# Kernel optimization log

Measured on AMD Instinct MI355X. Metric: run time of the kernel, lower is better.

The kernel has to match this reference:

```python
import jax, jax.numpy as jnp
import numpy as np

AUG_DIMS = 8
ODE_STEPS = 20  # fixed-step RK4 over t in [0, 1]


def _augment(x):
    # concat zeros along last (channel) dim: [B, S, F] -> [B, S, F + AUG_DIMS]
    z = jnp.zeros(x.shape[:-1] + (AUG_DIMS,), dtype=x.dtype)
    return jnp.concatenate([x, z], axis=-1)


def _ode_solve(z0, W, b):
    # dz/dt = z @ W.T + b, integrated with RK4, 20 steps, t: 0 -> 1
    h = 1.0 / ODE_STEPS

    def f(z):
        return z @ W.T + b

    def step(z, _):
        k1 = f(z)
        k2 = f(z + 0.5 * h * k1)
        k3 = f(z + 0.5 * h * k2)
        k4 = f(z + h * k3)
        z = z + (h / 6.0) * (k1 + 2.0 * k2 + 2.0 * k3 + k4)
        return z, None

    z_final, _ = jax.lax.scan(step, z0, None, length=ODE_STEPS)
    return z_final


def setup_inputs() -> dict:
    key = jax.random.key(0)
    ks = jax.random.split(key, 7)
    F_, C_, H_ = 76, 5, 128
    D = F_ + AUG_DIMS  # 84
    x = jax.random.normal(ks[0], (32, 2048, F_), dtype=jnp.float32)
    s = 1.0 / np.sqrt(D)
    W_ode = jax.random.uniform(ks[1], (D, D), minval=-s, maxval=s, dtype=jnp.float32)
    b_ode = jax.random.uniform(ks[2], (D,), minval=-s, maxval=s, dtype=jnp.float32)
    W_pen = jax.random.uniform(ks[3], (H_, D), minval=-s, maxval=s, dtype=jnp.float32)
    b_pen = jax.random.uniform(ks[4], (H_,), minval=-s, maxval=s, dtype=jnp.float32)
    sh = 1.0 / np.sqrt(H_)
    W_fin = jax.random.uniform(ks[5], (C_, H_), minval=-sh, maxval=sh, dtype=jnp.float32)
    b_fin = jax.random.uniform(ks[6], (C_,), minval=-sh, maxval=sh, dtype=jnp.float32)
    return {"x": x, "W_ode": W_ode, "b_ode": b_ode, "W_pen": W_pen,
            "b_pen": b_pen, "W_fin": W_fin, "b_fin": b_fin}


def reference(x, W_ode, b_ode, W_pen, b_pen, W_fin, b_fin):
    z0 = _augment(x)                       # [B, S, 84]
    z = _ode_solve(z0, W_ode, b_ode)       # ODE solve
    z = z + z0                             # skip-add of augmented input
    h = jax.nn.relu(z @ W_pen.T + b_pen)   # [B, S, 128]
    return h @ W_fin.T + b_fin             # [B, S, 5]
```

## Files before the change

### kernel.cpp

```cpp
#include <hip/hip_runtime.h>

#define K_IN 76
#define DD 84
#define HCH 128
#define CCH 5

#define OFF_U 0
#define OFF_C (K_IN*HCH)

__device__ __constant__ float CU[9] = {
    1.f, 0.5f, 1.f/6.f, 1.f/24.f, 1.f/120.f, 1.f/720.f, 1.f/5040.f,
    1.f/40320.f, 1.f/362880.f };
__device__ __constant__ float CC[9] = {
    0.5f, 1.f/6.f, 1.f/24.f, 1.f/120.f, 1.f/720.f, 1.f/5040.f,
    1.f/40320.f, 1.f/362880.f, 1.f/3628800.f };

__global__ __launch_bounds__(64, 1) void col_kernel(
    const float* __restrict__ W,
    const float* __restrict__ bode,
    const float* __restrict__ Wpen,
    const float* __restrict__ bpen,
    float* __restrict__ ws)
{
    __shared__ __align__(16) float Sa[88];
    __shared__ __align__(16) float Sb[88];

    const int l  = threadIdx.x;
    const int j  = blockIdx.x;
    const int i2 = 64 + l;
    const bool has2 = (l < 20);

    float wc1[DD], wc2[DD];
#pragma unroll
    for (int k = 0; k < DD; ++k) wc1[k] = W[k*DD + l];
    if (has2) {
#pragma unroll
        for (int k = 0; k < DD; ++k) wc2[k] = W[k*DD + i2];
    }

    float s1 = Wpen[j*DD + l];
    float s2 = has2 ? Wpen[j*DD + i2] : 0.f;
    const float b1 = bode[l];
    const float b2 = has2 ? bode[i2] : 0.f;

    Sa[l] = s1;
    if (has2) Sa[i2] = s2;
    __threadfence_block();

    float u1 = 2.f*s1, c1 = s1;
    float u2 = 2.f*s2, c2 = s2;

    const float* Sc = Sa;
    float*       Sn = Sb;
#pragma unroll
    for (int n = 0; n < 9; ++n) {
        float a0 = 0.f, a1 = 0.f, a2 = 0.f, a3 = 0.f;
        float e0 = 0.f, e1 = 0.f, e2 = 0.f, e3 = 0.f;
#pragma unroll
        for (int mg = 0; mg < 21; ++mg) {
            const float4 sv = *(const float4*)&Sc[mg*4];
            a0 = fmaf(sv.x, wc1[mg*4+0], a0);
            a1 = fmaf(sv.y, wc1[mg*4+1], a1);
            a2 = fmaf(sv.z, wc1[mg*4+2], a2);
            a3 = fmaf(sv.w, wc1[mg*4+3], a3);
            e0 = fmaf(sv.x, wc2[mg*4+0], e0);
            e1 = fmaf(sv.y, wc2[mg*4+1], e1);
            e2 = fmaf(sv.z, wc2[mg*4+2], e2);
            e3 = fmaf(sv.w, wc2[mg*4+3], e3);
        }
        const float d1 = (a0 + a1) + (a2 + a3);
        const float d2 = (e0 + e1) + (e2 + e3);

        Sn[l] = d1;
        if (has2) Sn[i2] = d2;
        __threadfence_block();

        u1 = fmaf(CU[n], d1, u1);  c1 = fmaf(CC[n], d1, c1);
        u2 = fmaf(CU[n], d2, u2);  c2 = fmaf(CC[n], d2, c2);

        float* t = (float*)Sc; Sc = Sn; Sn = t;
    }

    if (l < K_IN)            ws[OFF_U + l*HCH + j]  = u1;
    if (has2 && i2 < K_IN)   ws[OFF_U + i2*HCH + j] = u2;

    float cc = b1*c1 + b2*c2;
#pragma unroll
    for (int off = 32; off > 0; off >>= 1)
        cc += __shfl_down(cc, off, 64);
    if (l == 0) ws[OFF_C + j] = bpen[j] + cc;
}

__global__ __launch_bounds__(256) void main_kernel(
    const float* __restrict__ x,
    const float* __restrict__ Ug,
    const float* __restrict__ cg,
    const float* __restrict__ Wfin,
    const float* __restrict__ bfin,
    float* __restrict__ out)
{
    __shared__ float Ut[K_IN*HCH];
    __shared__ float xs[128*K_IN];
    __shared__ float Vl[CCH*HCH];

    const int tid = threadIdx.x;
    const int tx = tid & 31, ty = tid >> 5;
    const int T0 = blockIdx.x * 128;

    for (int i = tid; i < (K_IN*HCH)/4; i += 256)
        ((float4*)Ut)[i] = ((const float4*)Ug)[i];
    {
        const float4* xg = (const float4*)(x + (size_t)T0 * K_IN);
        for (int i = tid; i < (128*K_IN)/4; i += 256)
            ((float4*)xs)[i] = xg[i];
    }
    for (int i = tid; i < CCH*HCH; i += 256) Vl[i] = Wfin[i];
    __syncthreads();

    const int j0 = tx*4;
    const int tb = ty*16;
    float acc[16][4];
#pragma unroll
    for (int t = 0; t < 16; ++t)
#pragma unroll
        for (int q = 0; q < 4; ++q) acc[t][q] = 0.f;

    for (int kc = 0; kc < 19; ++kc) {
        const float4 u0 = *(const float4*)&Ut[(4*kc+0)*HCH + j0];
        const float4 u1 = *(const float4*)&Ut[(4*kc+1)*HCH + j0];
        const float4 u2 = *(const float4*)&Ut[(4*kc+2)*HCH + j0];
        const float4 u3 = *(const float4*)&Ut[(4*kc+3)*HCH + j0];
#pragma unroll
        for (int ti = 0; ti < 16; ++ti) {
            const float4 xv = *(const float4*)&xs[(tb+ti)*K_IN + 4*kc];
            acc[ti][0] = fmaf(xv.x, u0.x, acc[ti][0]);
            acc[ti][1] = fmaf(xv.x, u0.y, acc[ti][1]);
            acc[ti][2] = fmaf(xv.x, u0.z, acc[ti][2]);
            acc[ti][3] = fmaf(xv.x, u0.w, acc[ti][3]);
            acc[ti][0] = fmaf(xv.y, u1.x, acc[ti][0]);
            acc[ti][1] = fmaf(xv.y, u1.y, acc[ti][1]);
            acc[ti][2] = fmaf(xv.y, u1.z, acc[ti][2]);
            acc[ti][3] = fmaf(xv.y, u1.w, acc[ti][3]);
            acc[ti][0] = fmaf(xv.z, u2.x, acc[ti][0]);
            acc[ti][1] = fmaf(xv.z, u2.y, acc[ti][1]);
            acc[ti][2] = fmaf(xv.z, u2.z, acc[ti][2]);
            acc[ti][3] = fmaf(xv.z, u2.w, acc[ti][3]);
            acc[ti][0] = fmaf(xv.w, u3.x, acc[ti][0]);
            acc[ti][1] = fmaf(xv.w, u3.y, acc[ti][1]);
            acc[ti][2] = fmaf(xv.w, u3.z, acc[ti][2]);
            acc[ti][3] = fmaf(xv.w, u3.w, acc[ti][3]);
        }
    }

    const float4 cv = *(const float4*)&cg[j0];
    float* opp = xs;
    float* opf = Ut;
    __syncthreads();

    for (int tg = 0; tg < 4; ++tg) {
        float oa[20];
#pragma unroll
        for (int s = 0; s < 4; ++s) {
            const int ti = tg*4 + s;
            const float h0 = fmaxf(acc[ti][0] + cv.x, 0.f);
            const float h1 = fmaxf(acc[ti][1] + cv.y, 0.f);
            const float h2 = fmaxf(acc[ti][2] + cv.z, 0.f);
            const float h3 = fmaxf(acc[ti][3] + cv.w, 0.f);
#pragma unroll
            for (int m = 0; m < CCH; ++m)
                oa[s*5+m] = h0*Vl[m*HCH + j0]     + h1*Vl[m*HCH + j0 + 1]
                          + h2*Vl[m*HCH + j0 + 2] + h3*Vl[m*HCH + j0 + 3];
        }
#pragma unroll
        for (int i = 0; i < 20; ++i) opp[tid*21 + i] = oa[i];
        __syncthreads();
        if (tid < 160) {
            const int typ = tid / 20, rem = tid % 20;
            float s = 0.f;
            for (int xx = 0; xx < 32; ++xx)
                s += opp[(typ*32 + xx)*21 + rem];
            opf[(typ*16 + tg*4)*5 + rem] = s;
        }
        __syncthreads();
    }

    if (tid < 160) {
        const int gi = tid*4;
        float4 v = *(const float4*)&opf[gi];
        v.x += bfin[(gi+0) % 5]; v.y += bfin[(gi+1) % 5];
        v.z += bfin[(gi+2) % 5]; v.w += bfin[(gi+3) % 5];
        *(float4*)&out[(size_t)T0*CCH + gi] = v;
    }
}

extern "C" void kernel_launch(void* const* d_in, const int* in_sizes, int n_in,
                              void* d_out, int out_size, void* d_ws, size_t ws_size,
                              hipStream_t stream)
{
    (void)in_sizes; (void)n_in; (void)out_size; (void)ws_size;
    const float* x    = (const float*)d_in[0];
    const float* Wode = (const float*)d_in[1];
    const float* bode = (const float*)d_in[2];
    const float* Wpen = (const float*)d_in[3];
    const float* bpen = (const float*)d_in[4];
    const float* Wfin = (const float*)d_in[5];
    const float* bfin = (const float*)d_in[6];
    float* out = (float*)d_out;
    float* wsf = (float*)d_ws;

    col_kernel<<<dim3(HCH), dim3(64), 0, stream>>>(Wode, bode, Wpen, bpen, wsf);
    main_kernel<<<dim3(512), dim3(256), 0, stream>>>(x, wsf + OFF_U, wsf + OFF_C,
                                                     Wfin, bfin, out);
}
```

Baseline: 34.27 us.

## Fuse column precompute into main kernel with global flag spin-wait

Merges the column-precompute kernel into the main kernel. The first 128 blocks use one wave to compute the collapsed ODE+penultimate projection and signal completion through an atomic counter, while the other waves and blocks load their x tiles and wait on that flag. The Taylor series for the matrix exponential is also truncated from 9 to 7 terms, which cuts work but may lose accuracy. The change removes a kernel launch boundary and overlaps the x load with the precompute. In exchange it relies on all 512 blocks being co-resident, adds a memset, and puts a spin loop with a guard break on the critical path.

```diff
diff --git a/kernel.cpp b/kernel.cpp
--- a/kernel.cpp
+++ b/kernel.cpp
@@ -5,118 +5,132 @@
 #define HCH 128
 #define CCH 5
 
+#define NCOL 128
+#define NTILE 512
+
 #define OFF_U 0
 #define OFF_C (K_IN*HCH)
-
-__device__ __constant__ float CU[9] = {
-    1.f, 0.5f, 1.f/6.f, 1.f/24.f, 1.f/120.f, 1.f/720.f, 1.f/5040.f,
-    1.f/40320.f, 1.f/362880.f };
-__device__ __constant__ float CC[9] = {
-    0.5f, 1.f/6.f, 1.f/24.f, 1.f/120.f, 1.f/720.f, 1.f/5040.f,
-    1.f/40320.f, 1.f/362880.f, 1.f/3628800.f };
-
-__global__ __launch_bounds__(64, 1) void col_kernel(
+#define OFF_FLAG 9856
+
+__device__ __constant__ float CU7[7] = {
+    1.f, 0.5f, 1.f/6.f, 1.f/24.f, 1.f/120.f, 1.f/720.f, 1.f/5040.f };
+__device__ __constant__ float CC7[7] = {
+    0.5f, 1.f/6.f, 1.f/24.f, 1.f/120.f, 1.f/720.f, 1.f/5040.f, 1.f/40320.f };
+
+__global__ __launch_bounds__(256, 2) void fused_kernel(
+    const float* __restrict__ x,
     const float* __restrict__ W,
     const float* __restrict__ bode,
     const float* __restrict__ Wpen,
     const float* __restrict__ bpen,
-    float* __restrict__ ws)
-{
-    __shared__ __align__(16) float Sa[88];
-    __shared__ __align__(16) float Sb[88];
-
-    const int l  = threadIdx.x;
-    const int j  = blockIdx.x;
-    const int i2 = 64 + l;
-    const bool has2 = (l < 20);
-
-    float wc1[DD], wc2[DD];
-#pragma unroll
-    for (int k = 0; k < DD; ++k) wc1[k] = W[k*DD + l];
-    if (has2) {
-#pragma unroll
-        for (int k = 0; k < DD; ++k) wc2[k] = W[k*DD + i2];
-    }
-
-    float s1 = Wpen[j*DD + l];
-    float s2 = has2 ? Wpen[j*DD + i2] : 0.f;
-    const float b1 = bode[l];
-    const float b2 = has2 ? bode[i2] : 0.f;
-
-    Sa[l] = s1;
-    if (has2) Sa[i2] = s2;
-    __threadfence_block();
-
-    float u1 = 2.f*s1, c1 = s1;
-    float u2 = 2.f*s2, c2 = s2;
-
-    const float* Sc = Sa;
-    float*       Sn = Sb;
-#pragma unroll
-    for (int n = 0; n < 9; ++n) {
-        float a0 = 0.f, a1 = 0.f, a2 = 0.f, a3 = 0.f;
-        float e0 = 0.f, e1 = 0.f, e2 = 0.f, e3 = 0.f;
-#pragma unroll
-        for (int mg = 0; mg < 21; ++mg) {
-            const float4 sv = *(const float4*)&Sc[mg*4];
-            a0 = fmaf(sv.x, wc1[mg*4+0], a0);
-            a1 = fmaf(sv.y, wc1[mg*4+1], a1);
-            a2 = fmaf(sv.z, wc1[mg*4+2], a2);
-            a3 = fmaf(sv.w, wc1[mg*4+3], a3);
-            e0 = fmaf(sv.x, wc2[mg*4+0], e0);
-            e1 = fmaf(sv.y, wc2[mg*4+1], e1);
-            e2 = fmaf(sv.z, wc2[mg*4+2], e2);
-            e3 = fmaf(sv.w, wc2[mg*4+3], e3);
-        }
-        const float d1 = (a0 + a1) + (a2 + a3);
-        const float d2 = (e0 + e1) + (e2 + e3);
-
-        Sn[l] = d1;
-        if (has2) Sn[i2] = d2;
-        __threadfence_block();
-
-        u1 = fmaf(CU[n], d1, u1);  c1 = fmaf(CC[n], d1, c1);
-        u2 = fmaf(CU[n], d2, u2);  c2 = fmaf(CC[n], d2, c2);
-
-        float* t = (float*)Sc; Sc = Sn; Sn = t;
-    }
-
-    if (l < K_IN)            ws[OFF_U + l*HCH + j]  = u1;
-    if (has2 && i2 < K_IN)   ws[OFF_U + i2*HCH + j] = u2;
-
-    float cc = b1*c1 + b2*c2;
-#pragma unroll
-    for (int off = 32; off > 0; off >>= 1)
-        cc += __shfl_down(cc, off, 64);
-    if (l == 0) ws[OFF_C + j] = bpen[j] + cc;
-}
-
-__global__ __launch_bounds__(256) void main_kernel(
-    const float* __restrict__ x,
-    const float* __restrict__ Ug,
-    const float* __restrict__ cg,
     const float* __restrict__ Wfin,
     const float* __restrict__ bfin,
-    float* __restrict__ out)
+    float* __restrict__ out,
+    float* __restrict__ ws,
+    unsigned* __restrict__ flag)
 {
     __shared__ float Ut[K_IN*HCH];
     __shared__ float xs[128*K_IN];
     __shared__ float Vl[CCH*HCH];
 
     const int tid = threadIdx.x;
+    const int bid = blockIdx.x;
+    const bool iscol = (bid < NCOL);
+    const int wv = tid >> 6;
+    const int T0 = bid * 128;
+
+    if (iscol && wv == 0) {
+        float* Sa = Ut;
+        float* Sb = Ut + 96;
+        const int l  = tid;
+        const int i2 = 64 + l;
+        const bool has2 = (l < 20);
+
+        float wc1[DD], wc2[DD];
+#pragma unroll
+        for (int k = 0; k < DD; ++k) wc1[k] = W[k*DD + l];
+        if (has2) {
+#pragma unroll
+            for (int k = 0; k < DD; ++k) wc2[k] = W[k*DD + i2];
+        }
+        float s1 = Wpen[bid*DD + l];
+        float s2 = has2 ? Wpen[bid*DD + i2] : 0.f;
+        const float b1 = bode[l];
+        const float b2 = has2 ? bode[i2] : 0.f;
+
+        Sa[l] = s1; if (has2) Sa[i2] = s2;
+        __threadfence_block();
+
+        float u1 = 2.f*s1, c1 = s1;
+        float u2 = 2.f*s2, c2 = s2;
+        const float* Sc = Sa; float* Sn = Sb;
+#pragma unroll
+        for (int n = 0; n < 7; ++n) {
+            float a0=0.f,a1=0.f,a2=0.f,a3=0.f, e0=0.f,e1=0.f,e2=0.f,e3=0.f;
+#pragma unroll
+            for (int mg = 0; mg < 21; ++mg) {
+                const float4 sv = *(const float4*)&Sc[mg*4];
+                a0 = fmaf(sv.x, wc1[mg*4+0], a0);
+                a1 = fmaf(sv.y, wc1[mg*4+1], a1);
+                a2 = fmaf(sv.z, wc1[mg*4+2], a2);
+                a3 = fmaf(sv.w, wc1[mg*4+3], a3);
+                e0 = fmaf(sv.x, wc2[mg*4+0], e0);
+                e1 = fmaf(sv.y, wc2[mg*4+1], e1);
+                e2 = fmaf(sv.z, wc2[mg*4+2], e2);
+                e3 = fmaf(sv.w, wc2[mg*4+3], e3);
+            }
+            const float d1 = (a0+a1)+(a2+a3);
+            const float d2 = (e0+e1)+(e2+e3);
+            Sn[l] = d1; if (has2) Sn[i2] = d2;
+            __threadfence_block();
+            u1 = fmaf(CU7[n], d1, u1);  c1 = fmaf(CC7[n], d1, c1);
+            u2 = fmaf(CU7[n], d2, u2);  c2 = fmaf(CC7[n], d2, c2);
+            float* t = (float*)Sc; Sc = Sn; Sn = t;
+        }
+        if (l < K_IN)          ws[OFF_U + l*HCH + bid]  = u1;
+        if (has2 && i2 < K_IN) ws[OFF_U + i2*HCH + bid] = u2;
+
+        float cc = b1*c1 + (has2 ? b2*c2 : 0.f);
+#pragma unroll
+        for (int off = 32; off > 0; off >>= 1) cc += __shfl_down(cc, off, 64);
+        if (l == 0) {
+            ws[OFF_C + bid] = bpen[bid] + cc;
+            __threadfence();
+            __hip_atomic_fetch_add(flag, 1u, __ATOMIC_RELEASE,
+                                   __HIP_MEMORY_SCOPE_AGENT);
+        }
+    } else {
+        const int nst = iscol ? 192 : 256;
+        const int st  = iscol ? (tid - 64) : tid;
+        const float4* xg = (const float4*)(x + (size_t)T0 * K_IN);
+        for (int i = st; i < (128*K_IN)/4; i += nst)
+            ((float4*)xs)[i] = xg[i];
+        for (int i = st; i < CCH*HCH; i += nst) Vl[i] = Wfin[i];
+    }
+
+    {
+        float z0 = 1.0f + 1e-7f*(float)tid, z1 = z0 + 0.25f;
+        float z2 = z0 + 0.5f, z3 = z0 + 0.75f;
+        int guard = 0;
+        while (__hip_atomic_load(flag, __ATOMIC_ACQUIRE,
+                                 __HIP_MEMORY_SCOPE_AGENT) < NCOL) {
+#pragma unroll
+            for (int i = 0; i < 256; ++i) {
+                z0 = fmaf(z0, 1.0000001f, 1e-9f);
+                z1 = fmaf(z1, 1.0000001f, 1e-9f);
+                z2 = fmaf(z2, 1.0000001f, 1e-9f);
+                z3 = fmaf(z3, 1.0000001f, 1e-9f);
+            }
+            if (++guard > (1<<15)) break;
+        }
+        asm volatile("" :: "v"(z0), "v"(z1), "v"(z2), "v"(z3));
+    }
+
+    for (int i = tid; i < (K_IN*HCH)/4; i += 256)
+        ((float4*)Ut)[i] = ((const float4*)(ws + OFF_U))[i];
+    __syncthreads();
+
     const int tx = tid & 31, ty = tid >> 5;
-    const int T0 = blockIdx.x * 128;
-
-    for (int i = tid; i < (K_IN*HCH)/4; i += 256)
-        ((float4*)Ut)[i] = ((const float4*)Ug)[i];
-    {
-        const float4* xg = (const float4*)(x + (size_t)T0 * K_IN);
-        for (int i = tid; i < (128*K_IN)/4; i += 256)
-            ((float4*)xs)[i] = xg[i];
-    }
-    for (int i = tid; i < CCH*HCH; i += 256) Vl[i] = Wfin[i];
-    __syncthreads();
-
     const int j0 = tx*4;
     const int tb = ty*16;
     float acc[16][4];
@@ -152,7 +166,7 @@
         }
     }
 
-    const float4 cv = *(const float4*)&cg[j0];
+    const float4 cv = *(const float4*)&ws[OFF_C + j0];
     float* opp = xs;
     float* opf = Ut;
     __syncthreads();
@@ -207,8 +221,9 @@
     const float* bfin = (const float*)d_in[6];
     float* out = (float*)d_out;
     float* wsf = (float*)d_ws;
-
-    col_kernel<<<dim3(HCH), dim3(64), 0, stream>>>(Wode, bode, Wpen, bpen, wsf);
-    main_kernel<<<dim3(512), dim3(256), 0, stream>>>(x, wsf + OFF_U, wsf + OFF_C,
-                                                     Wfin, bfin, out);
+    unsigned* flag = (unsigned*)(wsf + OFF_FLAG);
+
+    hipMemsetAsync(flag, 0, 64, stream);
+    fused_kernel<<<dim3(NTILE), dim3(256), 0, stream>>>(
+        x, Wode, bode, Wpen, bpen, Wfin, bfin, out, wsf, flag);
 }
```

New measurement: 99.82 us. 2.91x slower.
